# Performance work log

Measured on AMD Instinct MI355X. Metric: run time of the kernel, lower is better.

The kernel has to match this reference:

```python
import jax, jax.numpy as jnp
import numpy as np

B, D, F = 32768, 512, 512  # batch, input features, output features (num_feats)


def setup_inputs() -> dict:
    key = jax.random.key(0)
    kx, kw, ka, kb = jax.random.split(key, 4)
    x = jax.random.normal(kx, (B, D), dtype=jnp.float32)
    W = jax.random.normal(kw, (F, D), dtype=jnp.float32) / np.float32(np.sqrt(D))
    a = jax.random.normal(ka, (F,), dtype=jnp.float32)
    b = jax.random.normal(kb, (F,), dtype=jnp.float32)
    return {"x": x, "W": W, "a": a, "b": b}


def reference(x, W, a, b):
    # Vectorized form of the nested map_fn:
    # out[i, f] = tanh(b[f] + a[f] * dot(W[f, :], x[i, :]))
    z = jnp.einsum('bd,fd->bf', x, W)  # [B, F] GEMM replacing per-(sample,feature) dots
    return jnp.tanh(a * z + b)
```

## Files before the change

### kernel.cpp

```cpp
#include <hip/hip_runtime.h>
#include <hip/hip_bf16.h>
#include <math.h>


typedef _Float16     f16x8 __attribute__((ext_vector_type(8)));
typedef float        f32x4 __attribute__((ext_vector_type(4)));
typedef unsigned int u32x2 __attribute__((ext_vector_type(2)));

static constexpr int Mdim = 32768;
static constexpr int Kdim = 512;
static constexpr int Ndim = 512;

__device__ __forceinline__ unsigned pk16(float a, float b) {
  union { _Float16 h; unsigned short u; } ca, cb;
  ca.h = (_Float16)a;
  cb.h = (_Float16)b;
  return (unsigned)ca.u | ((unsigned)cb.u << 16);
}

__device__ __forceinline__ float fast_tanh(float x) {
  float e = __expf(2.0f * x);
  return 1.0f - 2.0f * __builtin_amdgcn_rcpf(e + 1.0f);
}

__device__ __forceinline__ void glds16(const unsigned short* g, unsigned short* l) {
  __builtin_amdgcn_global_load_lds(
      (const __attribute__((address_space(1))) unsigned int*)g,
      (__attribute__((address_space(3))) unsigned int*)l, 16, 0, 0);
}

__global__ __launch_bounds__(256) void conv_w(const float* __restrict__ Wm,
                                              unsigned short* __restrict__ wh) {
  const int idx = blockIdx.x * 256 + threadIdx.x;
  f32x4 v = *(const f32x4*)(Wm + (size_t)idx * 4);
  u32x2 p = { pk16(v[0], v[1]), pk16(v[2], v[3]) };
  *(u32x2*)(wh + (size_t)idx * 4) = p;
}

__global__ __launch_bounds__(512, 4) void gemm_f16(
    const float* __restrict__ X, const unsigned short* __restrict__ Wh,
    const float* __restrict__ avec, const float* __restrict__ bvec,
    float* __restrict__ out) {
  __shared__ unsigned short lds[2][2][128 * 64];

  const int bid = blockIdx.x;
  const int vid = (bid & 7) * 128 + (bid >> 3);
  const int nB  = vid & 3;
  const int mB  = vid >> 2;
  const int tid  = threadIdx.x;
  const int lane = tid & 63;
  const int wid  = tid >> 6;
  const int wm = wid >> 2, wn = wid & 3;

  f32x4 acc[4][2];
#pragma unroll
  for (int i = 0; i < 4; ++i)
#pragma unroll
    for (int j = 0; j < 2; ++j) acc[i][j] = {0.f, 0.f, 0.f, 0.f};

  const int srow  = tid >> 4;
  const int scol4 = tid & 15;
  const int kcol  = scol4 * 4;
  const int soff0 = kcol >> 3;
  const float* Xb = X + (size_t)mB * 128 * Kdim;

  const int rl  = lane >> 3;
  const int ssl = (lane & 7) ^ rl;
  const int brow0 = nB * 128 + wid * 16 + rl;
  const unsigned short* sB0 = Wh + (size_t)brow0 * Kdim + ssl * 8;
  const unsigned short* sB1 = Wh + (size_t)(brow0 + 8) * Kdim + ssl * 8;

  glds16(sB0, &lds[0][1][(wid * 16) * 64]);
  glds16(sB1, &lds[0][1][(wid * 16 + 8) * 64]);
#pragma unroll
  for (int i = 0; i < 4; ++i) {
    const int row = srow + 32 * i;
    f32x4 r = *(const f32x4*)(Xb + (size_t)row * Kdim + kcol);
    const int off = row * 64 + ((soff0 ^ (row & 7)) << 3) + (kcol & 7);
    u32x2 p = { pk16(r[0], r[1]), pk16(r[2], r[3]) };
    *(u32x2*)&lds[0][0][off] = p;
  }
  __syncthreads();

  int cur = 0;
  for (int kt = 0; kt < Kdim / 64; ++kt) {
    const int nxt = cur ^ 1;
    f32x4 rA[4];
    if (kt < Kdim / 64 - 1) {
      const int kb = (kt + 1) * 64;
      glds16(sB0 + kb, &lds[nxt][1][(wid * 16) * 64]);
      glds16(sB1 + kb, &lds[nxt][1][(wid * 16 + 8) * 64]);
#pragma unroll
      for (int i = 0; i < 4; ++i)
        rA[i] = *(const f32x4*)(Xb + (size_t)(srow + 32 * i) * Kdim + kb + kcol);
    }

#pragma unroll
    for (int ks = 0; ks < 2; ++ks) {
      const int slotBase = ks * 4 + (lane >> 4);
      f16x8 bfr[2];
#pragma unroll
      for (int ni = 0; ni < 2; ++ni) {
        const int row = wn * 32 + ni * 16 + (lane & 15);
        const int off = row * 64 + ((slotBase ^ (row & 7)) << 3);
        bfr[ni] = *(const f16x8*)&lds[cur][1][off];
      }
#pragma unroll
      for (int mi = 0; mi < 4; ++mi) {
        const int row = wm * 64 + mi * 16 + (lane & 15);
        const int off = row * 64 + ((slotBase ^ (row & 7)) << 3);
        f16x8 afr = *(const f16x8*)&lds[cur][0][off];
#pragma unroll
        for (int ni = 0; ni < 2; ++ni)
          acc[mi][ni] = __builtin_amdgcn_mfma_f32_16x16x32_f16(afr, bfr[ni], acc[mi][ni], 0, 0, 0);
      }
    }

    if (kt < Kdim / 64 - 1) {
#pragma unroll
      for (int i = 0; i < 4; ++i) {
        const int row = srow + 32 * i;
        const int off = row * 64 + ((soff0 ^ (row & 7)) << 3) + (kcol & 7);
        u32x2 p = { pk16(rA[i][0], rA[i][1]), pk16(rA[i][2], rA[i][3]) };
        *(u32x2*)&lds[nxt][0][off] = p;
      }
    }
    __syncthreads();
    cur = nxt;
  }

  const int c  = lane & 15;
  const int rq = (lane >> 4) * 4;
#pragma unroll
  for (int ni = 0; ni < 2; ++ni) {
    const int gc = nB * 128 + wn * 32 + ni * 16 + c;
    const float aa = avec[gc];
    const float bb = bvec[gc];
#pragma unroll
    for (int mi = 0; mi < 4; ++mi) {
      const int gr = mB * 128 + wm * 64 + mi * 16 + rq;
      f32x4 v = acc[mi][ni];
#pragma unroll
      for (int j = 0; j < 4; ++j) {
        out[(size_t)(gr + j) * Ndim + gc] = fast_tanh(aa * v[j] + bb);
      }
    }
  }
}

typedef short bf16x8 __attribute__((ext_vector_type(8)));

__device__ __forceinline__ unsigned cvt_pk_bf16(float a, float b) {
  unsigned r;
  asm("v_cvt_pk_bf16_f32 %0, %1, %2" : "=v"(r) : "v"(a), "v"(b));
  return r;
}
__device__ __forceinline__ void split4(f32x4 v, u32x2& hi, u32x2& lo) {
  unsigned h0 = cvt_pk_bf16(v[0], v[1]);
  unsigned h1 = cvt_pk_bf16(v[2], v[3]);
  float f0 = __uint_as_float(h0 << 16);
  float f1 = __uint_as_float(h0 & 0xFFFF0000u);
  float f2 = __uint_as_float(h1 << 16);
  float f3 = __uint_as_float(h1 & 0xFFFF0000u);
  lo[0] = cvt_pk_bf16(v[0] - f0, v[1] - f1);
  lo[1] = cvt_pk_bf16(v[2] - f2, v[3] - f3);
  hi[0] = h0; hi[1] = h1;
}

__global__ __launch_bounds__(512, 4) void gemm_nows(
    const float* __restrict__ X, const float* __restrict__ Wm,
    const float* __restrict__ avec, const float* __restrict__ bvec,
    float* __restrict__ out) {
  __shared__ unsigned short lds[4][128 * 64];
  const int bid = blockIdx.x;
  const int nB  = bid & 3;
  const int mB  = bid >> 2;
  const int tid  = threadIdx.x;
  const int lane = tid & 63;
  const int wid  = tid >> 6;
  const int wm = wid >> 2, wn = wid & 3;

  f32x4 acc[4][2];
#pragma unroll
  for (int i = 0; i < 4; ++i)
#pragma unroll
    for (int j = 0; j < 2; ++j) acc[i][j] = {0.f, 0.f, 0.f, 0.f};

  const int srow  = tid >> 4;
  const int scol4 = tid & 15;
  const int kcol  = scol4 * 4;
  const int soff0 = kcol >> 3;
  const float* Xb = X  + (size_t)mB * 128 * Kdim;
  const float* Wb = Wm + (size_t)nB * 128 * Kdim;

  f32x4 rA[4], rB[4];
#pragma unroll
  for (int i = 0; i < 4; ++i) {
    const int row = srow + 32 * i;
    rA[i] = *(const f32x4*)(Xb + (size_t)row * Kdim + kcol);
    rB[i] = *(const f32x4*)(Wb + (size_t)row * Kdim + kcol);
  }
  for (int kt = 0; kt < Kdim / 64; ++kt) {
#pragma unroll
    for (int i = 0; i < 4; ++i) {
      const int row = srow + 32 * i;
      const int off = row * 64 + ((soff0 ^ (row & 7)) << 3) + (kcol & 7);
      u32x2 h, l;
      split4(rA[i], h, l);
      *(u32x2*)&lds[0][off] = h;
      *(u32x2*)&lds[1][off] = l;
      split4(rB[i], h, l);
      *(u32x2*)&lds[2][off] = h;
      *(u32x2*)&lds[3][off] = l;
    }
    __syncthreads();
    if (kt != Kdim / 64 - 1) {
      const int kbase = (kt + 1) * 64;
#pragma unroll
      for (int i = 0; i < 4; ++i) {
        const int row = srow + 32 * i;
        rA[i] = *(const f32x4*)(Xb + (size_t)row * Kdim + kbase + kcol);
        rB[i] = *(const f32x4*)(Wb + (size_t)row * Kdim + kbase + kcol);
      }
    }
#pragma unroll
    for (int ks = 0; ks < 2; ++ks) {
      const int slotBase = ks * 4 + (lane >> 4);
      bf16x8 bh[2], bl[2];
#pragma unroll
      for (int ni = 0; ni < 2; ++ni) {
        const int row = wn * 32 + ni * 16 + (lane & 15);
        const int off = row * 64 + ((slotBase ^ (row & 7)) << 3);
        bh[ni] = *(const bf16x8*)&lds[2][off];
        bl[ni] = *(const bf16x8*)&lds[3][off];
      }
#pragma unroll
      for (int mi = 0; mi < 4; ++mi) {
        const int row = wm * 64 + mi * 16 + (lane & 15);
        const int off = row * 64 + ((slotBase ^ (row & 7)) << 3);
        bf16x8 ah = *(const bf16x8*)&lds[0][off];
        bf16x8 al = *(const bf16x8*)&lds[1][off];
#pragma unroll
        for (int ni = 0; ni < 2; ++ni) {
          acc[mi][ni] = __builtin_amdgcn_mfma_f32_16x16x32_bf16(ah, bh[ni], acc[mi][ni], 0, 0, 0);
          acc[mi][ni] = __builtin_amdgcn_mfma_f32_16x16x32_bf16(ah, bl[ni], acc[mi][ni], 0, 0, 0);
          acc[mi][ni] = __builtin_amdgcn_mfma_f32_16x16x32_bf16(al, bh[ni], acc[mi][ni], 0, 0, 0);
        }
      }
    }
    __syncthreads();
  }
  const int c  = lane & 15;
  const int rq = (lane >> 4) * 4;
#pragma unroll
  for (int ni = 0; ni < 2; ++ni) {
    const int gc = nB * 128 + wn * 32 + ni * 16 + c;
    const float aa = avec[gc];
    const float bb = bvec[gc];
#pragma unroll
    for (int mi = 0; mi < 4; ++mi) {
      const int gr = mB * 128 + wm * 64 + mi * 16 + rq;
      f32x4 v = acc[mi][ni];
#pragma unroll
      for (int j = 0; j < 4; ++j) {
        out[(size_t)(gr + j) * Ndim + gc] = fast_tanh(aa * v[j] + bb);
      }
    }
  }
}

extern "C" void kernel_launch(void* const* d_in, const int* in_sizes, int n_in,
                              void* d_out, int out_size, void* d_ws, size_t ws_size,
                              hipStream_t stream) {
  const float* X  = (const float*)d_in[0];
  const float* Wm = (const float*)d_in[1];
  const float* av = (const float*)d_in[2];
  const float* bv = (const float*)d_in[3];
  float* out = (float*)d_out;

  const size_t wBytes = (size_t)Ndim * Kdim * sizeof(unsigned short);
  if (ws_size >= wBytes) {
    unsigned short* wh = (unsigned short*)d_ws;
    conv_w<<<dim3(Ndim * Kdim / 4 / 256), dim3(256), 0, stream>>>(Wm, wh);
    gemm_f16<<<dim3((Mdim / 128) * (Ndim / 128)), dim3(512), 0, stream>>>(X, wh, av, bv, out);
  } else {
    gemm_nows<<<dim3((Mdim / 128) * (Ndim / 128)), dim3(512), 0, stream>>>(X, Wm, av, bv, out);
  }
}
```

Before: 146.3 us.

## Keep full-K weight panel in LDS and stream X directly into registers

```diff
diff --git a/kernel.cpp b/kernel.cpp
--- a/kernel.cpp
+++ b/kernel.cpp
@@ -6,6 +6,7 @@
 typedef _Float16     f16x8 __attribute__((ext_vector_type(8)));
 typedef float        f32x4 __attribute__((ext_vector_type(4)));
 typedef unsigned int u32x2 __attribute__((ext_vector_type(2)));
+typedef unsigned int u32x4 __attribute__((ext_vector_type(4)));
 
 static constexpr int Mdim = 32768;
 static constexpr int Kdim = 512;
@@ -16,6 +17,13 @@
   ca.h = (_Float16)a;
   cb.h = (_Float16)b;
   return (unsigned)ca.u | ((unsigned)cb.u << 16);
+}
+
+__device__ __forceinline__ f16x8 pack8(f32x4 a, f32x4 b) {
+  u32x4 u = { pk16(a[0], a[1]), pk16(a[2], a[3]), pk16(b[0], b[1]), pk16(b[2], b[3]) };
+  union { u32x4 u; f16x8 h; } cv;
+  cv.u = u;
+  return cv.h;
 }
 
 __device__ __forceinline__ float fast_tanh(float x) {
@@ -37,108 +45,77 @@
   *(u32x2*)(wh + (size_t)idx * 4) = p;
 }
 
-__global__ __launch_bounds__(512, 4) void gemm_f16(
+__global__ __launch_bounds__(512, 4) void gemm_bpanel(
     const float* __restrict__ X, const unsigned short* __restrict__ Wh,
     const float* __restrict__ avec, const float* __restrict__ bvec,
     float* __restrict__ out) {
-  __shared__ unsigned short lds[2][2][128 * 64];
+  __shared__ unsigned short ldsB[64 * 512];
 
   const int bid = blockIdx.x;
   const int vid = (bid & 7) * 128 + (bid >> 3);
-  const int nB  = vid & 3;
-  const int mB  = vid >> 2;
+  const int nP  = vid & 7;
+  const int mC  = vid >> 3;
   const int tid  = threadIdx.x;
   const int lane = tid & 63;
   const int wid  = tid >> 6;
-  const int wm = wid >> 2, wn = wid & 3;
-
-  f32x4 acc[4][2];
-#pragma unroll
-  for (int i = 0; i < 4; ++i)
-#pragma unroll
-    for (int j = 0; j < 2; ++j) acc[i][j] = {0.f, 0.f, 0.f, 0.f};
-
-  const int srow  = tid >> 4;
-  const int scol4 = tid & 15;
-  const int kcol  = scol4 * 4;
-  const int soff0 = kcol >> 3;
-  const float* Xb = X + (size_t)mB * 128 * Kdim;
-
-  const int rl  = lane >> 3;
-  const int ssl = (lane & 7) ^ rl;
-  const int brow0 = nB * 128 + wid * 16 + rl;
-  const unsigned short* sB0 = Wh + (size_t)brow0 * Kdim + ssl * 8;
-  const unsigned short* sB1 = Wh + (size_t)(brow0 + 8) * Kdim + ssl * 8;
-
-  glds16(sB0, &lds[0][1][(wid * 16) * 64]);
-  glds16(sB1, &lds[0][1][(wid * 16 + 8) * 64]);
-#pragma unroll
-  for (int i = 0; i < 4; ++i) {
-    const int row = srow + 32 * i;
-    f32x4 r = *(const f32x4*)(Xb + (size_t)row * Kdim + kcol);
-    const int off = row * 64 + ((soff0 ^ (row & 7)) << 3) + (kcol & 7);
-    u32x2 p = { pk16(r[0], r[1]), pk16(r[2], r[3]) };
-    *(u32x2*)&lds[0][0][off] = p;
+
+#pragma unroll
+  for (int i = 0; i < 8; ++i) {
+    const int r = wid * 8 + i;
+    const int sigma = (lane & ~7) | ((lane & 7) ^ (r & 7));
+    glds16(Wh + (size_t)(nP * 64 + r) * Kdim + sigma * 8, &ldsB[r * 512]);
   }
   __syncthreads();
 
-  int cur = 0;
-  for (int kt = 0; kt < Kdim / 64; ++kt) {
-    const int nxt = cur ^ 1;
-    f32x4 rA[4];
-    if (kt < Kdim / 64 - 1) {
-      const int kb = (kt + 1) * 64;
-      glds16(sB0 + kb, &lds[nxt][1][(wid * 16) * 64]);
-      glds16(sB1 + kb, &lds[nxt][1][(wid * 16 + 8) * 64]);
-#pragma unroll
-      for (int i = 0; i < 4; ++i)
-        rA[i] = *(const f32x4*)(Xb + (size_t)(srow + 32 * i) * Kdim + kb + kcol);
-    }
-
-#pragma unroll
-    for (int ks = 0; ks < 2; ++ks) {
-      const int slotBase = ks * 4 + (lane >> 4);
-      f16x8 bfr[2];
-#pragma unroll
-      for (int ni = 0; ni < 2; ++ni) {
-        const int row = wn * 32 + ni * 16 + (lane & 15);
-        const int off = row * 64 + ((slotBase ^ (row & 7)) << 3);
-        bfr[ni] = *(const f16x8*)&lds[cur][1][off];
-      }
-#pragma unroll
-      for (int mi = 0; mi < 4; ++mi) {
-        const int row = wm * 64 + mi * 16 + (lane & 15);
-        const int off = row * 64 + ((slotBase ^ (row & 7)) << 3);
-        f16x8 afr = *(const f16x8*)&lds[cur][0][off];
-#pragma unroll
-        for (int ni = 0; ni < 2; ++ni)
-          acc[mi][ni] = __builtin_amdgcn_mfma_f32_16x16x32_f16(afr, bfr[ni], acc[mi][ni], 0, 0, 0);
-      }
-    }
-
-    if (kt < Kdim / 64 - 1) {
-#pragma unroll
-      for (int i = 0; i < 4; ++i) {
-        const int row = srow + 32 * i;
-        const int off = row * 64 + ((soff0 ^ (row & 7)) << 3) + (kcol & 7);
-        u32x2 p = { pk16(rA[i][0], rA[i][1]), pk16(rA[i][2], rA[i][3]) };
-        *(u32x2*)&lds[nxt][0][off] = p;
-      }
-    }
-    __syncthreads();
-    cur = nxt;
-  }
-
-  const int c  = lane & 15;
-  const int rq = (lane >> 4) * 4;
-#pragma unroll
-  for (int ni = 0; ni < 2; ++ni) {
-    const int gc = nB * 128 + wn * 32 + ni * 16 + c;
+  const int p = lane & 15;
+  const int q = lane >> 4;
+  const int rowBase = mC * 256 + wid * 32;
+  const float* Xl = X + (size_t)(rowBase + p) * Kdim + q * 8;
+
+  f32x4 acc[2][4];
+#pragma unroll
+  for (int i = 0; i < 2; ++i)
+#pragma unroll
+    for (int j = 0; j < 4; ++j) acc[i][j] = {0.f, 0.f, 0.f, 0.f};
+
+  f32x4 n0 = *(const f32x4*)(Xl);
+  f32x4 n1 = *(const f32x4*)(Xl + 4);
+  f32x4 n2 = *(const f32x4*)(Xl + 16 * Kdim);
+  f32x4 n3 = *(const f32x4*)(Xl + 16 * Kdim + 4);
+
+#pragma unroll
+  for (int t = 0; t < 16; ++t) {
+    f32x4 c0 = n0, c1 = n1, c2 = n2, c3 = n3;
+    if (t < 15) {
+      const int kb = (t + 1) * 32;
+      n0 = *(const f32x4*)(Xl + kb);
+      n1 = *(const f32x4*)(Xl + kb + 4);
+      n2 = *(const f32x4*)(Xl + 16 * Kdim + kb);
+      n3 = *(const f32x4*)(Xl + 16 * Kdim + kb + 4);
+    }
+    f16x8 af0 = pack8(c0, c1);
+    f16x8 af1 = pack8(c2, c3);
+
+    const int s = 4 * t + q;
+#pragma unroll
+    for (int ni = 0; ni < 4; ++ni) {
+      const int r   = ni * 16 + p;
+      const int off = r * 512 + ((s & ~7) | ((s & 7) ^ (p & 7))) * 8;
+      f16x8 bf = *(const f16x8*)&ldsB[off];
+      acc[0][ni] = __builtin_amdgcn_mfma_f32_16x16x32_f16(af0, bf, acc[0][ni], 0, 0, 0);
+      acc[1][ni] = __builtin_amdgcn_mfma_f32_16x16x32_f16(af1, bf, acc[1][ni], 0, 0, 0);
+    }
+  }
+
+  const int rq = q * 4;
+#pragma unroll
+  for (int ni = 0; ni < 4; ++ni) {
+    const int gc = nP * 64 + ni * 16 + p;
     const float aa = avec[gc];
     const float bb = bvec[gc];
 #pragma unroll
-    for (int mi = 0; mi < 4; ++mi) {
-      const int gr = mB * 128 + wm * 64 + mi * 16 + rq;
+    for (int mi = 0; mi < 2; ++mi) {
+      const int gr = rowBase + mi * 16 + rq;
       f32x4 v = acc[mi][ni];
 #pragma unroll
       for (int j = 0; j < 4; ++j) {
@@ -282,7 +259,7 @@
   if (ws_size >= wBytes) {
     unsigned short* wh = (unsigned short*)d_ws;
     conv_w<<<dim3(Ndim * Kdim / 4 / 256), dim3(256), 0, stream>>>(Wm, wh);
-    gemm_f16<<<dim3((Mdim / 128) * (Ndim / 128)), dim3(512), 0, stream>>>(X, wh, av, bv, out);
+    gemm_bpanel<<<dim3(1024), dim3(512), 0, stream>>>(X, wh, av, bv, out);
   } else {
     gemm_nows<<<dim3((Mdim / 128) * (Ndim / 128)), dim3(512), 0, stream>>>(X, Wm, av, bv, out);
   }
```

After: 172.3 us. +17.7%, slower.
